# Kernel tuning notes

Hardware: AMD Instinct MI355X
Metric: run time of the kernel (lower is better)

## Reference

```python
import math
import jax, jax.numpy as jnp
import numpy as np

B, L, D = 16, 2048, 64  # batch, seq len (m == n, self-attention), head dim
C = 30                   # ProbSparse sampling factor c


def setup_inputs() -> dict:
    key = jax.random.key(0)
    kq, kk, kv = jax.random.split(key, 3)
    Q = jax.random.normal(kq, (B, L, D), dtype=jnp.float32)
    K = jax.random.normal(kk, (B, L, D), dtype=jnp.float32)
    V = jax.random.normal(kv, (B, L, D), dtype=jnp.float32)
    return {"Q": Q, "K": K, "V": V, "seed": 0}


def reference(Q, K, V, seed):
    b, m, d = Q.shape
    n = K.shape[1]
    u = int(C * math.log(m))              # number of active queries
    U = min(int(m * math.log(n)), n)      # number of sampled keys (clamped to n)
    inv_sqrt_d = 1.0 / math.sqrt(d)

    rngs = jax.random.split(jax.random.key(seed), b)

    def _each_sample(Qb, Kb, Vb, r):
        # random sample of U key rows without replacement
        idx = jax.random.choice(r, n, shape=(U,), replace=False)
        Kbar = Kb[idx]                                # [U, d]
        Sbar = jnp.matmul(Qb, Kbar.T)                 # [m, U]
        M = jnp.max(Sbar, axis=1) - jnp.mean(Sbar, axis=1)  # sparsity measure [m]
        _, I = jax.lax.top_k(M, u)                    # active query indices [u]
        Qbar = Qb[I]                                  # [u, d]
        A = jax.nn.softmax(jnp.matmul(Qbar, Kb.T) * inv_sqrt_d, axis=-1)  # [u, n]
        S1 = jnp.matmul(A, Vb)                        # [u, d]
        # literal source: fill with mean(V, axis=1, keepdims=True) -> (n,1) broadcast (m==n)
        S = jnp.broadcast_to(jnp.mean(Vb, axis=1, keepdims=True), (m, d))
        return S.at[I].set(S1)

    return jax.vmap(_each_sample)(Q, K, V, rngs)
```

## Files before the change

kernel.cpp:

```cpp
#include <hip/hip_runtime.h>

#define NB 16
#define NN 2048
#define DH 64
#define NSEL 228
#define KS 8
#define CHUNK (NN / KS)
#define RS 4
#define EPSBAND 2.0e-3f
#define MAXB 32

using s16x8 = __attribute__((ext_vector_type(8))) short;
using f32x16 = __attribute__((ext_vector_type(16))) float;

static __device__ __forceinline__ unsigned short f2bf(float x) {
  unsigned int u = __float_as_uint(x);
  u += 0x7fffu + ((u >> 16) & 1u);
  return (unsigned short)(u >> 16);
}
static __device__ __forceinline__ float bf2f(unsigned short h) {
  return __uint_as_float(((unsigned int)h) << 16);
}
static __device__ __forceinline__ unsigned int enc(float f) {
  unsigned int u = __float_as_uint(f);
  return (u & 0x80000000u) ? ~u : (u | 0x80000000u);
}
static __device__ __forceinline__ float dec(unsigned int k) {
  return (k & 0x80000000u) ? __uint_as_float(k & 0x7fffffffu)
                           : __uint_as_float(~k);
}

__global__ __launch_bounds__(256) void convk_kernel(const float* __restrict__ K,
                                                    unsigned short* __restrict__ Khi,
                                                    unsigned short* __restrict__ Klo) {
  const size_t e = ((size_t)blockIdx.x * 256 + threadIdx.x) * 8;
  float4 a = *(const float4*)(K + e);
  float4 b = *(const float4*)(K + e + 4);
  float v[8] = {a.x, a.y, a.z, a.w, b.x, b.y, b.z, b.w};
  union { unsigned short u[8]; s16x8 s; } H, L;
  #pragma unroll
  for (int j = 0; j < 8; ++j) {
    unsigned short h = f2bf(v[j]);
    H.u[j] = h;
    L.u[j] = f2bf(v[j] - bf2f(h));
  }
  *(s16x8*)(Khi + e) = H.s;
  *(s16x8*)(Klo + e) = L.s;
}

__global__ __launch_bounds__(256) void kcolsum_kernel(const float* __restrict__ K,
                                                      float* __restrict__ Kpart) {
  __shared__ float part[4][64];
  const int b = blockIdx.y, ch = blockIdx.x;
  const int d = threadIdx.x & 63, g = threadIdx.x >> 6;
  const float* Kb = K + ((size_t)b * NN + ch * 128) * DH;
  float s = 0.f;
  for (int r = g; r < 128; r += 4) s += Kb[r * DH + d];
  part[g][d] = s;
  __syncthreads();
  if (threadIdx.x < 64)
    Kpart[((size_t)b * 16 + ch) * 64 + threadIdx.x] =
        part[0][threadIdx.x] + part[1][threadIdx.x] +
        part[2][threadIdx.x] + part[3][threadIdx.x];
}

__global__ __launch_bounds__(256, 4) void rowstat_mfma(const float* __restrict__ Q,
                                                       const unsigned short* __restrict__ Khi,
                                                       const unsigned short* __restrict__ Klo,
                                                       float* __restrict__ Mmax) {
  __shared__ __align__(16) unsigned short KHs[128 * 64];
  __shared__ __align__(16) unsigned short KLs[128 * 64];
  const int b = blockIdx.y, cz = blockIdx.z;
  const int qbase = blockIdx.x * 128;
  const int tid = threadIdx.x;
  const int w = tid >> 6, lane = tid & 63;
  const int l31 = lane & 31, hi5 = lane >> 5;

  s16x8 qh[4], ql[4];
  {
    const float* qrow = Q + ((size_t)b * NN + qbase + w * 32 + l31) * DH;
    #pragma unroll
    for (int ks = 0; ks < 4; ++ks) {
      const int d0 = ks * 16 + hi5 * 8;
      float4 x = *(const float4*)(qrow + d0);
      float4 y = *(const float4*)(qrow + d0 + 4);
      float v[8] = {x.x, x.y, x.z, x.w, y.x, y.y, y.z, y.w};
      union { unsigned short u[8]; s16x8 s; } H, L;
      #pragma unroll
      for (int j = 0; j < 8; ++j) {
        unsigned short h = f2bf(v[j]);
        H.u[j] = h;
        L.u[j] = f2bf(v[j] - bf2f(h));
      }
      qh[ks] = H.s;
      ql[ks] = L.s;
    }
  }

  const size_t kbase = ((size_t)b * NN + cz * (NN / RS)) * DH;
  f32x16 vmax;
  #pragma unroll
  for (int i = 0; i < 16; ++i) vmax[i] = -3.0e38f;

  const int sr = tid >> 1;
  const int sh = tid & 1;

  for (int stage = 0; stage < NN / RS / 128; ++stage) {
    __syncthreads();
    {
      const size_t g = kbase + (size_t)(stage * 128 + sr) * DH + sh * 32;
      const unsigned short* gh = Khi + g;
      const unsigned short* gl = Klo + g;
      #pragma unroll
      for (int c = 0; c < 4; ++c) {
        s16x8 hv = *(const s16x8*)(gh + c * 8);
        s16x8 lv = *(const s16x8*)(gl + c * 8);
        const int chn = (sh * 4 + c) ^ (sr & 7);
        *(s16x8*)&KHs[(sr * 8 + chn) * 8] = hv;
        *(s16x8*)&KLs[(sr * 8 + chn) * 8] = lv;
      }
    }
    __syncthreads();

    #pragma unroll
    for (int ksub = 0; ksub < 4; ++ksub) {
      const int kr = ksub * 32 + l31;
      f32x16 acc;
      #pragma unroll
      for (int i = 0; i < 16; ++i) acc[i] = 0.f;
      #pragma unroll
      for (int ks = 0; ks < 4; ++ks) {
        const int chn = (ks * 2 + hi5) ^ (kr & 7);
        s16x8 ah = *(const s16x8*)&KHs[(kr * 8 + chn) * 8];
        s16x8 al = *(const s16x8*)&KLs[(kr * 8 + chn) * 8];
        acc = __builtin_amdgcn_mfma_f32_32x32x16_bf16(ah, qh[ks], acc, 0, 0, 0);
        acc = __builtin_amdgcn_mfma_f32_32x32x16_bf16(al, qh[ks], acc, 0, 0, 0);
        acc = __builtin_amdgcn_mfma_f32_32x32x16_bf16(ah, ql[ks], acc, 0, 0, 0);
      }
      #pragma unroll
      for (int i = 0; i < 16; ++i) vmax[i] = fmaxf(vmax[i], acc[i]);
    }
  }

  float m = vmax[0];
  #pragma unroll
  for (int i = 1; i < 16; ++i) m = fmaxf(m, vmax[i]);
  m = fmaxf(m, __shfl_xor(m, 32));
  if (lane < 32)
    Mmax[((size_t)cz * NB + b) * NN + qbase + w * 32 + lane] = m;
}

__global__ __launch_bounds__(256) void mstat_kernel(const float* __restrict__ Q,
                                                    const float* __restrict__ Mmax,
                                                    const float* __restrict__ Kpart,
                                                    unsigned int* __restrict__ keysW,
                                                    float* __restrict__ meanv) {
  __shared__ float Ksl[64];
  const int b = blockIdx.y;
  const int seg = blockIdx.x;
  const int tid = threadIdx.x;
  if (tid < 64) {
    float s = 0.f;
    #pragma unroll
    for (int c = 0; c < 16; ++c) s += Kpart[((size_t)b * 16 + c) * 64 + tid];
    Ksl[tid] = s;
  }
  __syncthreads();
  const int i = seg * 256 + tid;
  float mv = -3.0e38f;
  #pragma unroll
  for (int cz = 0; cz < RS; ++cz)
    mv = fmaxf(mv, Mmax[((size_t)cz * NB + b) * NN + i]);
  const float* qrow = Q + ((size_t)b * NN + i) * DH;
  float s = 0.f;
  #pragma unroll
  for (int d4 = 0; d4 < 16; ++d4) {
    float4 qv = *(const float4*)(qrow + d4 * 4);
    s = fmaf(qv.x, Ksl[d4 * 4 + 0], s);
    s = fmaf(qv.y, Ksl[d4 * 4 + 1], s);
    s = fmaf(qv.z, Ksl[d4 * 4 + 2], s);
    s = fmaf(qv.w, Ksl[d4 * 4 + 3], s);
  }
  const float mean = s * (1.0f / NN);
  meanv[(size_t)b * NN + i] = mean;
  keysW[(size_t)b * NN + i] = enc(mv - mean);
}

static __device__ unsigned int radix_thresh(const unsigned int* kreg, int lane,
                                            int wid, int* red) {
  unsigned int v = 0u;
  for (int bit = 31; bit >= 0; --bit) {
    const unsigned int cand = v | (1u << bit);
    int c = 0;
    #pragma unroll
    for (int f = 0; f < 8; ++f) c += (kreg[f] >= cand) ? 1 : 0;
    #pragma unroll
    for (int off = 1; off < 64; off <<= 1) c += __shfl_xor(c, off);
    if (lane == 0) red[wid] = c;
    __syncthreads();
    if (red[0] + red[1] + red[2] + red[3] >= NSEL) v = cand;
    __syncthreads();
  }
  return v;
}

__global__ __launch_bounds__(256) void radix1_kernel(const unsigned int* __restrict__ keysW,
                                                     int* __restrict__ Band,
                                                     int* __restrict__ nband) {
  __shared__ int red[4];
  __shared__ int cntS;
  const int b = blockIdx.x;
  const int tid = threadIdx.x;
  const int lane = tid & 63, wid = tid >> 6;
  const int base = tid * 8;

  unsigned int kreg[8];
  #pragma unroll
  for (int f = 0; f < 8; ++f) kreg[f] = keysW[(size_t)b * NN + base + f];
  if (tid == 0) cntS = 0;
  __syncthreads();

  const unsigned int v1 = radix_thresh(kreg, lane, wid, red);
  const float vf = dec(v1);

  #pragma unroll
  for (int f = 0; f < 8; ++f) {
    if (fabsf(dec(kreg[f]) - vf) <= EPSBAND) {
      int p = atomicAdd(&cntS, 1);
      Band[(size_t)b * NN + p] = base + f;
    }
  }
  __syncthreads();
  if (tid == 0) nband[b] = cntS;
}

__global__ __launch_bounds__(256) void recheck_kernel(const float* __restrict__ Q,
                                                      const float* __restrict__ K,
                                                      const int* __restrict__ Band,
                                                      const int* __restrict__ nband,
                                                      const float* __restrict__ meanv,
                                                      unsigned int* __restrict__ keysW) {
  __shared__ float qsh[64];
  __shared__ float fred[4];
  const int b = blockIdx.y;
  const int nb_ = nband[b];
  const int tid = threadIdx.x;
  const int lane = tid & 63, wid = tid >> 6;

  for (int n = blockIdx.x; n < nb_; n += MAXB) {
    const int row = Band[(size_t)b * NN + n];
    __syncthreads();
    if (tid < 64) qsh[tid] = Q[((size_t)b * NN + row) * DH + tid];
    __syncthreads();
    float lmax = -3.0e38f;
    for (int j = tid; j < NN; j += 256) {
      const float* krow = K + ((size_t)b * NN + j) * DH;
      float s = 0.f;
      #pragma unroll
      for (int d4 = 0; d4 < 16; ++d4) {
        float4 kv = *(const float4*)(krow + d4 * 4);
        s = fmaf(kv.x, qsh[d4 * 4 + 0], s);
        s = fmaf(kv.y, qsh[d4 * 4 + 1], s);
        s = fmaf(kv.z, qsh[d4 * 4 + 2], s);
        s = fmaf(kv.w, qsh[d4 * 4 + 3], s);
      }
      lmax = fmaxf(lmax, s);
    }
    #pragma unroll
    for (int off = 1; off < 64; off <<= 1)
      lmax = fmaxf(lmax, __shfl_xor(lmax, off));
    if (lane == 0) fred[wid] = lmax;
    __syncthreads();
    if (tid == 0) {
      const float mx = fmaxf(fmaxf(fred[0], fred[1]), fmaxf(fred[2], fred[3]));
      keysW[(size_t)b * NN + row] = enc(mx - meanv[(size_t)b * NN + row]);
    }
  }
}

__global__ __launch_bounds__(256) void radix2_kernel(const unsigned int* __restrict__ keysW,
                                                     int* __restrict__ Isel) {
  __shared__ int red[4];
  const int b = blockIdx.x;
  const int tid = threadIdx.x;
  const int lane = tid & 63, wid = tid >> 6;
  const int base = tid * 8;

  unsigned int kreg[8];
  #pragma unroll
  for (int f = 0; f < 8; ++f) kreg[f] = keysW[(size_t)b * NN + base + f];
  __syncthreads();

  const unsigned int v2 = radix_thresh(kreg, lane, wid, red);

  int flg[8];
  int cnt = 0;
  #pragma unroll
  for (int f = 0; f < 8; ++f) { flg[f] = (kreg[f] > v2) ? 1 : 0; cnt += flg[f]; }
  int scan = cnt;
  #pragma unroll
  for (int off = 1; off < 64; off <<= 1) {
    const int t = __shfl_up(scan, off);
    if (lane >= off) scan += t;
  }
  if (lane == 63) red[wid] = scan;
  __syncthreads();
  int wbase = 0;
  for (int ww = 0; ww < wid; ++ww) wbase += red[ww];
  const int cg = red[0] + red[1] + red[2] + red[3];
  int pos = wbase + scan - cnt;
  #pragma unroll
  for (int f = 0; f < 8; ++f)
    if (flg[f]) { Isel[b * NSEL + pos] = base + f; ++pos; }
  __syncthreads();

  const int need = NSEL - cg;
  cnt = 0;
  #pragma unroll
  for (int f = 0; f < 8; ++f) { flg[f] = (kreg[f] == v2) ? 1 : 0; cnt += flg[f]; }
  scan = cnt;
  #pragma unroll
  for (int off = 1; off < 64; off <<= 1) {
    const int t = __shfl_up(scan, off);
    if (lane >= off) scan += t;
  }
  if (lane == 63) red[wid] = scan;
  __syncthreads();
  wbase = 0;
  for (int ww = 0; ww < wid; ++ww) wbase += red[ww];
  pos = wbase + scan - cnt;
  #pragma unroll
  for (int f = 0; f < 8; ++f)
    if (flg[f]) {
      if (pos < need) Isel[b * NSEL + cg + pos] = base + f;
      ++pos;
    }
}

__global__ __launch_bounds__(256) void fill_kernel(const float* __restrict__ V,
                                                   float* __restrict__ out) {
  const size_t row = (size_t)blockIdx.x * 4 + (threadIdx.x >> 6);
  const int lane = threadIdx.x & 63;
  float x = V[row * DH + lane];
  #pragma unroll
  for (int off = 1; off < 64; off <<= 1) x += __shfl_xor(x, off);
  out[row * DH + lane] = x * (1.0f / DH);
}

__global__ __launch_bounds__(256) void attn_part_kernel(const float* __restrict__ Q,
                                                        const float* __restrict__ K,
                                                        const float* __restrict__ V,
                                                        const int* __restrict__ Isel,
                                                        float* __restrict__ Pm,
                                                        float* __restrict__ Pl,
                                                        float* __restrict__ Po) {
  __shared__ float Qt[64][32];
  __shared__ float Kt[64][64];
  __shared__ float Vs[64][64];
  __shared__ float Pt[64][36];
  const int b = blockIdx.z;
  const int kc = blockIdx.y;
  const int g = blockIdx.x;
  const int tid = threadIdx.x;
  const int wq = tid >> 5;
  const int kx = tid & 31;

  if (tid < 128) {
    const int rr = tid >> 2;
    const int dblk = (tid & 3) * 16;
    const int lq = g * 32 + rr;
    const int qidx = (lq < NSEL) ? Isel[b * NSEL + lq] : 0;
    const float* qs = Q + ((size_t)b * NN + qidx) * DH + dblk;
    #pragma unroll
    for (int f = 0; f < 4; ++f) {
      float4 v = *reinterpret_cast<const float4*>(qs + f * 4);
      Qt[dblk + f * 4 + 0][rr] = v.x;
      Qt[dblk + f * 4 + 1][rr] = v.y;
      Qt[dblk + f * 4 + 2][rr] = v.z;
      Qt[dblk + f * 4 + 3][rr] = v.w;
    }
  }

  const float* Kb = K + ((size_t)b * NN + kc * CHUNK) * DH;
  const float* Vb = V + ((size_t)b * NN + kc * CHUNK) * DH;

  float m[4], lp[4], o[4][2];
  #pragma unroll
  for (int a = 0; a < 4; ++a) {
    m[a] = -3.0e38f; lp[a] = 0.f; o[a][0] = 0.f; o[a][1] = 0.f;
  }

  for (int st = 0; st < CHUNK / 64; ++st) {
    __syncthreads();
    {
      const int rr = tid & 63;
      const int dblk = (tid >> 6) * 16;
      const float* ks = Kb + ((size_t)(st * 64 + rr)) * DH + dblk;
      #pragma unroll
      for (int f = 0; f < 4; ++f) {
        float4 v = *reinterpret_cast<const float4*>(ks + f * 4);
        Kt[dblk + f * 4 + 0][rr] = v.x;
        Kt[dblk + f * 4 + 1][rr] = v.y;
        Kt[dblk + f * 4 + 2][rr] = v.z;
        Kt[dblk + f * 4 + 3][rr] = v.w;
      }
      const float* vsrc = Vb + (size_t)st * 64 * DH;
      float* vdst = &Vs[0][0];
      #pragma unroll
      for (int it = 0; it < 4; ++it) {
        const int fo = (it * 256 + tid) * 4;
        *reinterpret_cast<float4*>(vdst + fo) =
            *reinterpret_cast<const float4*>(vsrc + fo);
      }
    }
    __syncthreads();

    float sc[4][2];
    #pragma unroll
    for (int a = 0; a < 4; ++a) { sc[a][0] = 0.f; sc[a][1] = 0.f; }
    #pragma unroll 4
    for (int d = 0; d < 64; ++d) {
      float qv[4];
      *reinterpret_cast<float4*>(qv) =
          *reinterpret_cast<const float4*>(&Qt[d][wq * 4]);
      const float2 kv = *reinterpret_cast<const float2*>(&Kt[d][kx * 2]);
      #pragma unroll
      for (int a = 0; a < 4; ++a) {
        sc[a][0] = fmaf(qv[a], kv.x, sc[a][0]);
        sc[a][1] = fmaf(qv[a], kv.y, sc[a][1]);
      }
    }
    #pragma unroll
    for (int a = 0; a < 4; ++a) { sc[a][0] *= 0.125f; sc[a][1] *= 0.125f; }

    float tm[4];
    #pragma unroll
    for (int a = 0; a < 4; ++a) tm[a] = fmaxf(sc[a][0], sc[a][1]);
    #pragma unroll
    for (int off = 1; off < 32; off <<= 1) {
      #pragma unroll
      for (int a = 0; a < 4; ++a) tm[a] = fmaxf(tm[a], __shfl_xor(tm[a], off));
    }

    float w0[4], w1[4];
    #pragma unroll
    for (int a = 0; a < 4; ++a) {
      const float mn = fmaxf(m[a], tm[a]);
      const float scale = __expf(m[a] - mn);
      m[a] = mn;
      lp[a] *= scale;
      o[a][0] *= scale;
      o[a][1] *= scale;
      w0[a] = __expf(sc[a][0] - mn);
      w1[a] = __expf(sc[a][1] - mn);
      lp[a] += w0[a] + w1[a];
    }
    *reinterpret_cast<float4*>(&Pt[kx * 2][wq * 4]) =
        make_float4(w0[0], w0[1], w0[2], w0[3]);
    *reinterpret_cast<float4*>(&Pt[kx * 2 + 1][wq * 4]) =
        make_float4(w1[0], w1[1], w1[2], w1[3]);
    __syncthreads();

    #pragma unroll 4
    for (int k = 0; k < 64; ++k) {
      float pv[4];
      *reinterpret_cast<float4*>(pv) =
          *reinterpret_cast<const float4*>(&Pt[k][wq * 4]);
      const float2 vv = *reinterpret_cast<const float2*>(&Vs[k][kx * 2]);
      #pragma unroll
      for (int a = 0; a < 4; ++a) {
        o[a][0] = fmaf(pv[a], vv.x, o[a][0]);
        o[a][1] = fmaf(pv[a], vv.y, o[a][1]);
      }
    }
  }

  #pragma unroll
  for (int off = 1; off < 32; off <<= 1) {
    #pragma unroll
    for (int a = 0; a < 4; ++a) lp[a] += __shfl_xor(lp[a], off);
  }

  #pragma unroll
  for (int a = 0; a < 4; ++a) {
    const int lq = g * 32 + wq * 4 + a;
    if (lq < NSEL) {
      const size_t row = ((size_t)b * NSEL + lq) * KS + kc;
      if (kx == 0) { Pm[row] = m[a]; Pl[row] = lp[a]; }
      *reinterpret_cast<float2*>(Po + row * 64 + kx * 2) =
          make_float2(o[a][0], o[a][1]);
    }
  }
}

__global__ __launch_bounds__(256) void combine_kernel(const int* __restrict__ Isel,
                                                      const float* __restrict__ Pm,
                                                      const float* __restrict__ Pl,
                                                      const float* __restrict__ Po,
                                                      float* __restrict__ out) {
  const int r = blockIdx.x * 4 + (threadIdx.x >> 6);
  if (r >= NB * NSEL) return;
  const int lane = threadIdx.x & 63;
  const int b = r / NSEL;
  const int qidx = Isel[r];
  const size_t base = (size_t)r * KS;

  float pm[KS];
  float gm = -3.0e38f;
  #pragma unroll
  for (int c = 0; c < KS; ++c) { pm[c] = Pm[base + c]; gm = fmaxf(gm, pm[c]); }
  float L = 0.f, od = 0.f;
  #pragma unroll
  for (int c = 0; c < KS; ++c) {
    const float e = __expf(pm[c] - gm);
    L += Pl[base + c] * e;
    od += Po[(base + c) * 64 + lane] * e;
  }
  out[((size_t)b * NN + qidx) * DH + lane] = od / L;
}

extern "C" void kernel_launch(void* const* d_in, const int* in_sizes, int n_in,
                              void* d_out, int out_size, void* d_ws, size_t ws_size,
                              hipStream_t stream) {
  const float* Q = (const float*)d_in[0];
  const float* K = (const float*)d_in[1];
  const float* V = (const float*)d_in[2];
  float* out = (float*)d_out;

  float* Mmax = (float*)d_ws;
  float* Kpart = Mmax + (size_t)RS * NB * NN;
  unsigned int* keysW = (unsigned int*)(Kpart + (size_t)NB * 16 * 64);
  float* meanv = (float*)(keysW + (size_t)NB * NN);
  int* Band = (int*)(meanv + (size_t)NB * NN);
  int* nband = Band + (size_t)NB * NN;
  int* Isel = nband + 16;
  float* Pm = (float*)(Isel + NB * NSEL);
  float* Pl = Pm + (size_t)NB * NSEL * KS;
  float* Po = Pl + (size_t)NB * NSEL * KS;
  unsigned short* Khi = (unsigned short*)(Po + (size_t)NB * NSEL * KS * 64);
  unsigned short* Klo = Khi + (size_t)NB * NN * DH;

  convk_kernel<<<dim3((NB * NN * DH) / (256 * 8)), 256, 0, stream>>>(K, Khi, Klo);
  kcolsum_kernel<<<dim3(16, NB), 256, 0, stream>>>(K, Kpart);
  rowstat_mfma<<<dim3(NN / 128, NB, RS), 256, 0, stream>>>(Q, Khi, Klo, Mmax);
  mstat_kernel<<<dim3(8, NB), 256, 0, stream>>>(Q, Mmax, Kpart, keysW, meanv);
  radix1_kernel<<<dim3(NB), 256, 0, stream>>>(keysW, Band, nband);
  recheck_kernel<<<dim3(MAXB, NB), 256, 0, stream>>>(Q, K, Band, nband, meanv, keysW);
  radix2_kernel<<<dim3(NB), 256, 0, stream>>>(keysW, Isel);
  fill_kernel<<<dim3(NB * NN / 4), 256, 0, stream>>>(V, out);
  attn_part_kernel<<<dim3(8, KS, NB), 256, 0, stream>>>(Q, K, V, Isel, Pm, Pl, Po);
  combine_kernel<<<dim3((NB * NSEL + 3) / 4), 256, 0, stream>>>(Isel, Pm, Pl, Po, out);
}
```

Before: 248.5 us.

## Move selected-query attention to split-bf16 MFMA with transposed V copy

Replaces the FP32 scalar-FMA attention partial kernel with an MFMA version. It uses a three-product hi/lo bf16 split for QK^T and PV, reusing the existing Khi/Klo buffers plus a new kernel that transposes V and splits it into bf16 hi/lo. Each wave handles 64 keys of the 256-key chunk with a single-pass softmax, and the four waves' partial outputs are reduced through LDS. This aims to cut the FP32 FMA cost and the shared-memory staging loop, at the price of an extra conversion kernel, more workspace, and a small loss of precision from the split.

```diff
diff --git a/kernel.cpp b/kernel.cpp
--- a/kernel.cpp
+++ b/kernel.cpp
@@ -46,6 +46,45 @@
   }
   *(s16x8*)(Khi + e) = H.s;
   *(s16x8*)(Klo + e) = L.s;
+}
+
+__global__ __launch_bounds__(256) void convv_kernel(const float* __restrict__ V,
+                                                    unsigned short* __restrict__ VThi,
+                                                    unsigned short* __restrict__ VTlo) {
+  __shared__ __align__(16) float T[64][65];
+  const int b = blockIdx.y, ch = blockIdx.x;
+  const int tid = threadIdx.x;
+  {
+    const int r = tid >> 2;
+    const int c0 = (tid & 3) * 16;
+    const float* src = V + ((size_t)b * NN + ch * 64 + r) * DH + c0;
+    #pragma unroll
+    for (int f = 0; f < 4; ++f) {
+      float4 v = *(const float4*)(src + f * 4);
+      T[r][c0 + f * 4 + 0] = v.x;
+      T[r][c0 + f * 4 + 1] = v.y;
+      T[r][c0 + f * 4 + 2] = v.z;
+      T[r][c0 + f * 4 + 3] = v.w;
+    }
+  }
+  __syncthreads();
+  const int d = tid >> 2;
+  const int j0 = (tid & 3) * 16;
+  unsigned short* oh = VThi + ((size_t)b * DH + d) * NN + ch * 64 + j0;
+  unsigned short* ol = VTlo + ((size_t)b * DH + d) * NN + ch * 64 + j0;
+  #pragma unroll
+  for (int half = 0; half < 2; ++half) {
+    union { unsigned short u[8]; s16x8 s; } H, L;
+    #pragma unroll
+    for (int c = 0; c < 8; ++c) {
+      const float v = T[j0 + half * 8 + c][d];
+      const unsigned short hh = f2bf(v);
+      H.u[c] = hh;
+      L.u[c] = f2bf(v - bf2f(hh));
+    }
+    *(s16x8*)(oh + half * 8) = H.s;
+    *(s16x8*)(ol + half * 8) = L.s;
+  }
 }
 
 __global__ __launch_bounds__(256) void kcolsum_kernel(const float* __restrict__ K,
@@ -347,148 +386,169 @@
   out[row * DH + lane] = x * (1.0f / DH);
 }
 
-__global__ __launch_bounds__(256) void attn_part_kernel(const float* __restrict__ Q,
-                                                        const float* __restrict__ K,
-                                                        const float* __restrict__ V,
-                                                        const int* __restrict__ Isel,
-                                                        float* __restrict__ Pm,
-                                                        float* __restrict__ Pl,
-                                                        float* __restrict__ Po) {
-  __shared__ float Qt[64][32];
-  __shared__ float Kt[64][64];
-  __shared__ float Vs[64][64];
-  __shared__ float Pt[64][36];
-  const int b = blockIdx.z;
-  const int kc = blockIdx.y;
-  const int g = blockIdx.x;
-  const int tid = threadIdx.x;
-  const int wq = tid >> 5;
-  const int kx = tid & 31;
-
-  if (tid < 128) {
-    const int rr = tid >> 2;
-    const int dblk = (tid & 3) * 16;
-    const int lq = g * 32 + rr;
-    const int qidx = (lq < NSEL) ? Isel[b * NSEL + lq] : 0;
-    const float* qs = Q + ((size_t)b * NN + qidx) * DH + dblk;
-    #pragma unroll
-    for (int f = 0; f < 4; ++f) {
-      float4 v = *reinterpret_cast<const float4*>(qs + f * 4);
-      Qt[dblk + f * 4 + 0][rr] = v.x;
-      Qt[dblk + f * 4 + 1][rr] = v.y;
-      Qt[dblk + f * 4 + 2][rr] = v.z;
-      Qt[dblk + f * 4 + 3][rr] = v.w;
-    }
-  }
-
-  const float* Kb = K + ((size_t)b * NN + kc * CHUNK) * DH;
-  const float* Vb = V + ((size_t)b * NN + kc * CHUNK) * DH;
-
-  float m[4], lp[4], o[4][2];
-  #pragma unroll
-  for (int a = 0; a < 4; ++a) {
-    m[a] = -3.0e38f; lp[a] = 0.f; o[a][0] = 0.f; o[a][1] = 0.f;
-  }
-
-  for (int st = 0; st < CHUNK / 64; ++st) {
-    __syncthreads();
-    {
-      const int rr = tid & 63;
-      const int dblk = (tid >> 6) * 16;
-      const float* ks = Kb + ((size_t)(st * 64 + rr)) * DH + dblk;
+__global__ __launch_bounds__(256, 2) void attn_mfma(const float* __restrict__ Q,
+                                                    const unsigned short* __restrict__ Khi,
+                                                    const unsigned short* __restrict__ Klo,
+                                                    const unsigned short* __restrict__ VThi,
+                                                    const unsigned short* __restrict__ VTlo,
+                                                    const int* __restrict__ Isel,
+                                                    float* __restrict__ Pm,
+                                                    float* __restrict__ Pl,
+                                                    float* __restrict__ Po) {
+  __shared__ float wmax[4][32];
+  __shared__ float wl[4][32];
+  __shared__ __align__(16) float Opart[4][32][68];
+  const int b = blockIdx.z, kc = blockIdx.y, g = blockIdx.x;
+  const int tid = threadIdx.x, w = tid >> 6, lane = tid & 63;
+  const int l31 = lane & 31, h = lane >> 5;
+
+  const int lq = g * 32 + l31;
+  const int qidx = (lq < NSEL) ? Isel[b * NSEL + lq] : Isel[b * NSEL];
+  s16x8 qbh[4], qbl[4];
+  {
+    const float* qr = Q + ((size_t)b * NN + qidx) * DH;
+    #pragma unroll
+    for (int s = 0; s < 4; ++s) {
+      const int d0 = s * 16 + h * 8;
+      float4 x = *(const float4*)(qr + d0);
+      float4 y = *(const float4*)(qr + d0 + 4);
+      float v[8] = {x.x, x.y, x.z, x.w, y.x, y.y, y.z, y.w};
+      union { unsigned short u[8]; s16x8 s8; } H, L;
       #pragma unroll
-      for (int f = 0; f < 4; ++f) {
-        float4 v = *reinterpret_cast<const float4*>(ks + f * 4);
-        Kt[dblk + f * 4 + 0][rr] = v.x;
-        Kt[dblk + f * 4 + 1][rr] = v.y;
-        Kt[dblk + f * 4 + 2][rr] = v.z;
-        Kt[dblk + f * 4 + 3][rr] = v.w;
+      for (int j = 0; j < 8; ++j) {
+        const unsigned short hh = f2bf(v[j]);
+        H.u[j] = hh;
+        L.u[j] = f2bf(v[j] - bf2f(hh));
       }
-      const float* vsrc = Vb + (size_t)st * 64 * DH;
-      float* vdst = &Vs[0][0];
-      #pragma unroll
-      for (int it = 0; it < 4; ++it) {
-        const int fo = (it * 256 + tid) * 4;
-        *reinterpret_cast<float4*>(vdst + fo) =
-            *reinterpret_cast<const float4*>(vsrc + fo);
-      }
-    }
-    __syncthreads();
-
-    float sc[4][2];
-    #pragma unroll
-    for (int a = 0; a < 4; ++a) { sc[a][0] = 0.f; sc[a][1] = 0.f; }
-    #pragma unroll 4
-    for (int d = 0; d < 64; ++d) {
-      float qv[4];
-      *reinterpret_cast<float4*>(qv) =
-          *reinterpret_cast<const float4*>(&Qt[d][wq * 4]);
-      const float2 kv = *reinterpret_cast<const float2*>(&Kt[d][kx * 2]);
-      #pragma unroll
-      for (int a = 0; a < 4; ++a) {
-        sc[a][0] = fmaf(qv[a], kv.x, sc[a][0]);
-        sc[a][1] = fmaf(qv[a], kv.y, sc[a][1]);
-      }
-    }
-    #pragma unroll
-    for (int a = 0; a < 4; ++a) { sc[a][0] *= 0.125f; sc[a][1] *= 0.125f; }
-
-    float tm[4];
-    #pragma unroll
-    for (int a = 0; a < 4; ++a) tm[a] = fmaxf(sc[a][0], sc[a][1]);
-    #pragma unroll
-    for (int off = 1; off < 32; off <<= 1) {
-      #pragma unroll
-      for (int a = 0; a < 4; ++a) tm[a] = fmaxf(tm[a], __shfl_xor(tm[a], off));
-    }
-
-    float w0[4], w1[4];
-    #pragma unroll
-    for (int a = 0; a < 4; ++a) {
-      const float mn = fmaxf(m[a], tm[a]);
-      const float scale = __expf(m[a] - mn);
-      m[a] = mn;
-      lp[a] *= scale;
-      o[a][0] *= scale;
-      o[a][1] *= scale;
-      w0[a] = __expf(sc[a][0] - mn);
-      w1[a] = __expf(sc[a][1] - mn);
-      lp[a] += w0[a] + w1[a];
-    }
-    *reinterpret_cast<float4*>(&Pt[kx * 2][wq * 4]) =
-        make_float4(w0[0], w0[1], w0[2], w0[3]);
-    *reinterpret_cast<float4*>(&Pt[kx * 2 + 1][wq * 4]) =
-        make_float4(w1[0], w1[1], w1[2], w1[3]);
-    __syncthreads();
-
-    #pragma unroll 4
-    for (int k = 0; k < 64; ++k) {
-      float pv[4];
-      *reinterpret_cast<float4*>(pv) =
-          *reinterpret_cast<const float4*>(&Pt[k][wq * 4]);
-      const float2 vv = *reinterpret_cast<const float2*>(&Vs[k][kx * 2]);
-      #pragma unroll
-      for (int a = 0; a < 4; ++a) {
-        o[a][0] = fmaf(pv[a], vv.x, o[a][0]);
-        o[a][1] = fmaf(pv[a], vv.y, o[a][1]);
-      }
-    }
-  }
-
-  #pragma unroll
-  for (int off = 1; off < 32; off <<= 1) {
-    #pragma unroll
-    for (int a = 0; a < 4; ++a) lp[a] += __shfl_xor(lp[a], off);
-  }
-
-  #pragma unroll
-  for (int a = 0; a < 4; ++a) {
-    const int lq = g * 32 + wq * 4 + a;
-    if (lq < NSEL) {
-      const size_t row = ((size_t)b * NSEL + lq) * KS + kc;
-      if (kx == 0) { Pm[row] = m[a]; Pl[row] = lp[a]; }
-      *reinterpret_cast<float2*>(Po + row * 64 + kx * 2) =
-          make_float2(o[a][0], o[a][1]);
+      qbh[s] = H.s8;
+      qbl[s] = L.s8;
+    }
+  }
+
+  const size_t krow0 = (size_t)b * NN + kc * CHUNK + w * 64;
+  f32x16 p[2];
+  #pragma unroll
+  for (int t = 0; t < 2; ++t) {
+    const unsigned short* kh = Khi + (krow0 + t * 32 + l31) * DH + h * 8;
+    const unsigned short* kl = Klo + (krow0 + t * 32 + l31) * DH + h * 8;
+    f32x16 acc;
+    #pragma unroll
+    for (int i = 0; i < 16; ++i) acc[i] = 0.f;
+    #pragma unroll
+    for (int s = 0; s < 4; ++s) {
+      const s16x8 ah = *(const s16x8*)(kh + s * 16);
+      const s16x8 al = *(const s16x8*)(kl + s * 16);
+      acc = __builtin_amdgcn_mfma_f32_32x32x16_bf16(ah, qbh[s], acc, 0, 0, 0);
+      acc = __builtin_amdgcn_mfma_f32_32x32x16_bf16(al, qbh[s], acc, 0, 0, 0);
+      acc = __builtin_amdgcn_mfma_f32_32x32x16_bf16(ah, qbl[s], acc, 0, 0, 0);
+    }
+    p[t] = acc;
+  }
+
+  float rmax = p[0][0];
+  #pragma unroll
+  for (int i = 1; i < 16; ++i) rmax = fmaxf(rmax, p[0][i]);
+  #pragma unroll
+  for (int i = 0; i < 16; ++i) rmax = fmaxf(rmax, p[1][i]);
+  rmax = fmaxf(rmax, __shfl_xor(rmax, 32));
+  if (lane < 32) wmax[w][lane] = rmax;
+  __syncthreads();
+  const float gmax = fmaxf(fmaxf(wmax[0][l31], wmax[1][l31]),
+                           fmaxf(wmax[2][l31], wmax[3][l31]));
+  const float m = gmax * 0.125f;
+
+  float lsum = 0.f;
+  #pragma unroll
+  for (int t = 0; t < 2; ++t)
+    #pragma unroll
+    for (int i = 0; i < 16; ++i) {
+      const float e = __expf(fmaf(p[t][i], 0.125f, -m));
+      p[t][i] = e;
+      lsum += e;
+    }
+  lsum += __shfl_xor(lsum, 32);
+  if (lane < 32) wl[w][lane] = lsum;
+
+  f32x16 oacc[2];
+  #pragma unroll
+  for (int i = 0; i < 16; ++i) { oacc[0][i] = 0.f; oacc[1][i] = 0.f; }
+
+  #pragma unroll
+  for (int s = 0; s < 4; ++s) {
+    const int t = s >> 1, kb = s & 1;
+    float pr[8];
+    #pragma unroll
+    for (int j = 0; j < 8; ++j) pr[j] = p[t][kb * 8 + j];
+    unsigned int ah[4], al[4];
+    #pragma unroll
+    for (int pi = 0; pi < 4; ++pi) {
+      const unsigned short h0 = f2bf(pr[pi * 2]);
+      const unsigned short h1 = f2bf(pr[pi * 2 + 1]);
+      ah[pi] = (unsigned int)h0 | ((unsigned int)h1 << 16);
+      al[pi] = (unsigned int)f2bf(pr[pi * 2] - bf2f(h0)) |
+               ((unsigned int)f2bf(pr[pi * 2 + 1] - bf2f(h1)) << 16);
+    }
+    unsigned int sh_[4], sl_[4];
+    #pragma unroll
+    for (int pi = 0; pi < 4; ++pi) {
+      sh_[pi] = (unsigned int)__shfl_xor((int)ah[pi], 32);
+      sl_[pi] = (unsigned int)__shfl_xor((int)al[pi], 32);
+    }
+    union { int4 i4; s16x8 s8; } BH, BL;
+    if (h == 0) {
+      BH.i4 = make_int4((int)ah[0], (int)ah[1], (int)sh_[0], (int)sh_[1]);
+      BL.i4 = make_int4((int)al[0], (int)al[1], (int)sl_[0], (int)sl_[1]);
+    } else {
+      BH.i4 = make_int4((int)sh_[2], (int)sh_[3], (int)ah[2], (int)ah[3]);
+      BL.i4 = make_int4((int)sl_[2], (int)sl_[3], (int)al[2], (int)al[3]);
+    }
+    const size_t koff = (size_t)kc * CHUNK + w * 64 + s * 16 + h * 8;
+    #pragma unroll
+    for (int dt = 0; dt < 2; ++dt) {
+      const size_t vrow = ((size_t)b * DH + dt * 32 + l31) * NN + koff;
+      const s16x8 av = *(const s16x8*)(VThi + vrow);
+      const s16x8 avl = *(const s16x8*)(VTlo + vrow);
+      oacc[dt] = __builtin_amdgcn_mfma_f32_32x32x16_bf16(av, BH.s8, oacc[dt], 0, 0, 0);
+      oacc[dt] = __builtin_amdgcn_mfma_f32_32x32x16_bf16(av, BL.s8, oacc[dt], 0, 0, 0);
+      oacc[dt] = __builtin_amdgcn_mfma_f32_32x32x16_bf16(avl, BH.s8, oacc[dt], 0, 0, 0);
+    }
+  }
+
+  #pragma unroll
+  for (int dt = 0; dt < 2; ++dt)
+    #pragma unroll
+    for (int rg = 0; rg < 4; ++rg) {
+      const int d0 = dt * 32 + rg * 8 + h * 4;
+      float4 vv;
+      vv.x = oacc[dt][rg * 4 + 0];
+      vv.y = oacc[dt][rg * 4 + 1];
+      vv.z = oacc[dt][rg * 4 + 2];
+      vv.w = oacc[dt][rg * 4 + 3];
+      *(float4*)&Opart[w][l31][d0] = vv;
+    }
+  __syncthreads();
+
+  const int q = tid >> 3, dg = (tid & 7) * 8;
+  float4 s0, s1;
+  s0.x = s0.y = s0.z = s0.w = 0.f;
+  s1.x = s1.y = s1.z = s1.w = 0.f;
+  #pragma unroll
+  for (int ww = 0; ww < 4; ++ww) {
+    const float4 a = *(const float4*)&Opart[ww][q][dg];
+    const float4 c = *(const float4*)&Opart[ww][q][dg + 4];
+    s0.x += a.x; s0.y += a.y; s0.z += a.z; s0.w += a.w;
+    s1.x += c.x; s1.y += c.y; s1.z += c.z; s1.w += c.w;
+  }
+  const int lq2 = g * 32 + q;
+  if (lq2 < NSEL) {
+    const size_t row = ((size_t)b * NSEL + lq2) * KS + kc;
+    *(float4*)(Po + row * 64 + dg) = s0;
+    *(float4*)(Po + row * 64 + dg + 4) = s1;
+    if (dg == 0) {
+      const float gm2 = fmaxf(fmaxf(wmax[0][q], wmax[1][q]),
+                              fmaxf(wmax[2][q], wmax[3][q]));
+      Pm[row] = gm2 * 0.125f;
+      Pl[row] = wl[0][q] + wl[1][q] + wl[2][q] + wl[3][q];
     }
   }
 }
@@ -539,8 +599,11 @@
   float* Po = Pl + (size_t)NB * NSEL * KS;
   unsigned short* Khi = (unsigned short*)(Po + (size_t)NB * NSEL * KS * 64);
   unsigned short* Klo = Khi + (size_t)NB * NN * DH;
+  unsigned short* VThi = Klo + (size_t)NB * NN * DH;
+  unsigned short* VTlo = VThi + (size_t)NB * NN * DH;
 
   convk_kernel<<<dim3((NB * NN * DH) / (256 * 8)), 256, 0, stream>>>(K, Khi, Klo);
+  convv_kernel<<<dim3(NN / 64, NB), 256, 0, stream>>>(V, VThi, VTlo);
   kcolsum_kernel<<<dim3(16, NB), 256, 0, stream>>>(K, Kpart);
   rowstat_mfma<<<dim3(NN / 128, NB, RS), 256, 0, stream>>>(Q, Khi, Klo, Mmax);
   mstat_kernel<<<dim3(8, NB), 256, 0, stream>>>(Q, Mmax, Kpart, keysW, meanv);
@@ -548,6 +611,7 @@
   recheck_kernel<<<dim3(MAXB, NB), 256, 0, stream>>>(Q, K, Band, nband, meanv, keysW);
   radix2_kernel<<<dim3(NB), 256, 0, stream>>>(keysW, Isel);
   fill_kernel<<<dim3(NB * NN / 4), 256, 0, stream>>>(V, out);
-  attn_part_kernel<<<dim3(8, KS, NB), 256, 0, stream>>>(Q, K, V, Isel, Pm, Pl, Po);
+  attn_mfma<<<dim3(8, KS, NB), 256, 0, stream>>>(Q, Khi, Klo, VThi, VTlo, Isel,
+                                                 Pm, Pl, Po);
   combine_kernel<<<dim3((NB * NSEL + 3) / 4), 256, 0, stream>>>(Isel, Pm, Pl, Po, out);
 }
```

Result: faster. 230.2 us (-7.4%).
